# Performance work log

Measured on AMD Instinct MI355X. Metric: run time of the kernel, lower is better.

Reference implementation:

```python
import jax, jax.numpy as jnp
import numpy as np

BN_EPS = 1e-5
KEEP_RATIO = 0.25
MIN_TOPK = 4


def setup_inputs() -> dict:
    key = jax.random.key(0)
    ks = jax.random.split(key, 8)
    B, C, H, W, HID = 32, 768, 32, 32, 96
    x = jax.random.normal(ks[0], (B, C, H, W), dtype=jnp.float32)
    # fan-in scaled weights so score magnitudes stay sane for softmax
    w1 = jax.random.normal(ks[1], (HID, C, 1, 1), dtype=jnp.float32) / np.sqrt(C)
    bn_gamma = jax.random.uniform(ks[2], (HID,), dtype=jnp.float32) + 0.5
    bn_beta = jax.random.normal(ks[3], (HID,), dtype=jnp.float32) * 0.1
    bn_mean = jax.random.normal(ks[4], (HID,), dtype=jnp.float32) * 0.1
    bn_var = jax.random.uniform(ks[5], (HID,), dtype=jnp.float32) + 0.5
    w2 = jax.random.normal(ks[6], (1, HID, 3, 3), dtype=jnp.float32) / np.sqrt(HID * 9)
    b2 = jax.random.normal(ks[7], (1,), dtype=jnp.float32) * 0.1
    return {"x": x, "w1": w1, "bn_gamma": bn_gamma, "bn_beta": bn_beta,
            "bn_mean": bn_mean, "bn_var": bn_var, "w2": w2, "b2": b2}


def reference(x, w1, bn_gamma, bn_beta, bn_mean, bn_var, w2, b2):
    B, C, H, W = x.shape
    N = H * W
    # 1x1 conv (no bias) as channel contraction: [B,C,H,W] x [HID,C] -> [B,HID,H,W]
    h = jnp.einsum('bchw,oc->bohw', x, w1[:, :, 0, 0])
    # BatchNorm in inference mode (running stats)
    scale = (bn_gamma / jnp.sqrt(bn_var + BN_EPS))[None, :, None, None]
    h = h * scale + (bn_beta - bn_mean * bn_gamma / jnp.sqrt(bn_var + BN_EPS))[None, :, None, None]
    h = jax.nn.relu(h)
    # 3x3 conv HID -> 1, padding=1
    score = jax.lax.conv_general_dilated(
        h, w2, window_strides=(1, 1), padding='SAME',
        dimension_numbers=('NCHW', 'OIHW', 'NCHW')) + b2[None, :, None, None]
    s = score.reshape(B, N)
    K = min(max(MIN_TOPK, int(N * KEEP_RATIO)), N)
    top_vals, top_idx = jax.lax.top_k(s, K)  # [B,K] (sorted; weighted sum is order-invariant)
    x_flat = x.reshape(B, C, N)
    sel = jnp.take_along_axis(x_flat, top_idx[:, None, :], axis=2)  # [B,C,K]
    w = jax.nn.softmax(top_vals, axis=1)[:, None, :]               # [B,1,K]
    v = jnp.sum(sel * w, axis=2)                                    # [B,C]
    # dropout p=0.0 -> identity
    return v, score.reshape(B, 1, H, W)
```

## Files before the change

kernel.cpp:

```cpp
#include <hip/hip_runtime.h>
#include <math.h>

#define BB 32
#define CC 768
#define HID 96
#define NPIX 1024
#define KSEL 256
#define BN_EPS_F 1e-5f

typedef __bf16 bf16x8 __attribute__((ext_vector_type(8)));
typedef float f32x4 __attribute__((ext_vector_type(4)));

__device__ __forceinline__ unsigned short f2bf(float f) {
    unsigned u = __float_as_uint(f);
    return (unsigned short)((u + 0x7FFFu + ((u >> 16) & 1u)) >> 16);
}
__device__ __forceinline__ unsigned pack2(float lo, float hi) {
    return (unsigned)f2bf(lo) | ((unsigned)f2bf(hi) << 16);
}

__global__ __launch_bounds__(256) void k0_prep(
    const float* __restrict__ w1, const float* __restrict__ gamma,
    const float* __restrict__ beta, const float* __restrict__ mean,
    const float* __restrict__ var,
    unsigned short* __restrict__ w1b, float* __restrict__ scale,
    float* __restrict__ shift)
{
    int t = threadIdx.x, bk = blockIdx.x;
    if (bk < 72) {
        int idx = (bk * 256 + t) * 4;
        float4 v = *reinterpret_cast<const float4*>(w1 + idx);
        uint2 o;
        o.x = pack2(v.x, v.y);
        o.y = pack2(v.z, v.w);
        *reinterpret_cast<uint2*>(w1b + idx) = o;
    } else if (t < HID) {
        float sc = gamma[t] * rsqrtf(var[t] + BN_EPS_F);
        scale[t] = sc;
        shift[t] = beta[t] - mean[t] * sc;
    }
}

__global__ __launch_bounds__(512, 4) void k1_gemm_mfma(
    const float* __restrict__ x, const unsigned short* __restrict__ w1b,
    const float* __restrict__ scale, const float* __restrict__ shift,
    float* __restrict__ h_out)
{
    __shared__ unsigned Xs[2][32][66];
    __shared__ unsigned short Ws[2][96][68];
    __shared__ float sc_s[HID], sh_s[HID];

    const int t = threadIdx.x;
    const int b = blockIdx.y;
    const int n0 = blockIdx.x * 64;
    const int wave = t >> 6, lane = t & 63;
    const int lm = lane & 15, g = lane >> 4;
    const int wo = wave >> 2, wn = wave & 3;
    const int nB = wn * 16 + lm;
    const int kp = t >> 4, q = t & 15;
    const int nc = q * 4;
    const int wrow = t >> 3, wko = (t & 7) * 8;
    const int wrow2 = (t + 512) >> 3, wko2 = wko;

    if (t < HID) { sc_s[t] = scale[t]; sh_s[t] = shift[t]; }

    f32x4 acc[3];
#pragma unroll
    for (int mt = 0; mt < 3; ++mt) acc[mt] = (f32x4){0.f, 0.f, 0.f, 0.f};

    const float* xbase = x + (size_t)b * CC * NPIX + n0;

    {
        const float* r0 = xbase + (size_t)(2 * kp) * NPIX;
        float4 a4 = *reinterpret_cast<const float4*>(r0 + nc);
        float4 b4 = *reinterpret_cast<const float4*>(r0 + NPIX + nc);
        uint4 pk;
        pk.x = pack2(a4.x, b4.x); pk.y = pack2(a4.y, b4.y);
        pk.z = pack2(a4.z, b4.z); pk.w = pack2(a4.w, b4.w);
        *reinterpret_cast<uint4*>(&Xs[0][kp][nc]) = pk;

        uint4 w0 = *reinterpret_cast<const uint4*>(w1b + (size_t)wrow * CC + wko);
        *reinterpret_cast<uint4*>(&Ws[0][wrow][wko]) = w0;
        if (t < 256) {
            uint4 w1v = *reinterpret_cast<const uint4*>(w1b + (size_t)wrow2 * CC + wko2);
            *reinterpret_cast<uint4*>(&Ws[0][wrow2][wko2]) = w1v;
        }
    }
    __syncthreads();

    int cur = 0;
#pragma unroll 1
    for (int c0 = 0; c0 < CC; c0 += 64) {
        const bool hasNext = (c0 + 64 < CC);
        float4 a4, b4;
        uint4 nw0, nw1;
        if (hasNext) {
            const float* r0 = xbase + (size_t)(c0 + 64 + 2 * kp) * NPIX;
            a4 = *reinterpret_cast<const float4*>(r0 + nc);
            b4 = *reinterpret_cast<const float4*>(r0 + NPIX + nc);
            nw0 = *reinterpret_cast<const uint4*>(
                w1b + (size_t)wrow * CC + c0 + 64 + wko);
            if (t < 256)
                nw1 = *reinterpret_cast<const uint4*>(
                    w1b + (size_t)wrow2 * CC + c0 + 64 + wko2);
        }
#pragma unroll
        for (int h = 0; h < 2; ++h) {
            uint4 bu;
            bu.x = Xs[cur][16 * h + 4 * g + 0][nB];
            bu.y = Xs[cur][16 * h + 4 * g + 1][nB];
            bu.z = Xs[cur][16 * h + 4 * g + 2][nB];
            bu.w = Xs[cur][16 * h + 4 * g + 3][nB];
            bf16x8 bfr = __builtin_bit_cast(bf16x8, bu);
#pragma unroll
            for (int mt = 0; mt < 3; ++mt) {
                uint4 au = *reinterpret_cast<const uint4*>(
                    &Ws[cur][wo * 48 + mt * 16 + lm][h * 32 + g * 8]);
                acc[mt] = __builtin_amdgcn_mfma_f32_16x16x32_bf16(
                    __builtin_bit_cast(bf16x8, au), bfr, acc[mt], 0, 0, 0);
            }
        }
        if (hasNext) {
            uint4 pk;
            pk.x = pack2(a4.x, b4.x); pk.y = pack2(a4.y, b4.y);
            pk.z = pack2(a4.z, b4.z); pk.w = pack2(a4.w, b4.w);
            *reinterpret_cast<uint4*>(&Xs[cur ^ 1][kp][nc]) = pk;
            *reinterpret_cast<uint4*>(&Ws[cur ^ 1][wrow][wko]) = nw0;
            if (t < 256)
                *reinterpret_cast<uint4*>(&Ws[cur ^ 1][wrow2][wko2]) = nw1;
        }
        __syncthreads();
        cur ^= 1;
    }

#pragma unroll
    for (int mt = 0; mt < 3; ++mt) {
#pragma unroll
        for (int r = 0; r < 4; ++r) {
            int o = wo * 48 + mt * 16 + g * 4 + r;
            float v = fmaxf(acc[mt][r] * sc_s[o] + sh_s[o], 0.f);
            h_out[((size_t)b * HID + o) * NPIX + n0 + nB] = v;
        }
    }
}

__global__ __launch_bounds__(128) void k2_conv3x3(
    const float* __restrict__ h_in, const float* __restrict__ w2,
    const float* __restrict__ b2, float* __restrict__ score_out)
{
    __shared__ float hs[16][6][40];
    __shared__ float w2s[HID * 9];

    const int t = threadIdx.x;
    const int ytile = blockIdx.x, b = blockIdx.y;
    const int y = t >> 5, xx = t & 31;
    const int Y = ytile * 4 + y;

    for (int i = t; i < HID * 9; i += 128) w2s[i] = w2[i];

    const float* hb = h_in + (size_t)b * HID * NPIX;
    float acc = 0.f;

    for (int c0 = 0; c0 < HID; c0 += 16) {
        __syncthreads();
        for (int i = t; i < 192; i += 128) {
            int ch = i / 12, rr = (i % 12) >> 1, col = (i & 1) ? 36 : 3;
            hs[ch][rr][col] = 0.f;
        }
#pragma unroll
        for (int i = 0; i < 6; ++i) {
            int idx = t + i * 128;
            int ch = idx / 48, rem = idx % 48;
            int rr = rem >> 3, qq = rem & 7;
            int gy = ytile * 4 - 1 + rr;
            float4 v = (gy >= 0 && gy < 32)
                ? *reinterpret_cast<const float4*>(
                      hb + (size_t)(c0 + ch) * NPIX + gy * 32 + qq * 4)
                : (float4){0.f, 0.f, 0.f, 0.f};
            *reinterpret_cast<float4*>(&hs[ch][rr][4 + qq * 4]) = v;
        }
        __syncthreads();
#pragma unroll
        for (int ch = 0; ch < 16; ++ch) {
            float s = 0.f;
#pragma unroll
            for (int ky = 0; ky < 3; ++ky)
#pragma unroll
                for (int kx = 0; kx < 3; ++kx)
                    s += hs[ch][y + ky][3 + xx + kx] * w2s[(c0 + ch) * 9 + ky * 3 + kx];
            acc += s;
        }
    }
    score_out[b * NPIX + Y * 32 + xx] = acc + b2[0];
}

__global__ __launch_bounds__(256) void k3_topk_softmax(
    const float* __restrict__ score, float* __restrict__ weight)
{
    __shared__ unsigned hist[256];
    __shared__ unsigned wtot[4];
    __shared__ unsigned pcnt16[16];
    __shared__ float redf[4];
    __shared__ unsigned sh_bin, sh_rem;

    const int t = threadIdx.x, b = blockIdx.x;
    const int lane = t & 63, wv = t >> 6;

    float fvals[4];
    unsigned uvals[4];
#pragma unroll
    for (int i = 0; i < 4; ++i) {
        float f = score[b * NPIX + t + 256 * i];
        fvals[i] = f;
        unsigned u = __float_as_uint(f);
        uvals[i] = (u & 0x80000000u) ? ~u : (u | 0x80000000u);
    }

    unsigned prefix = 0, rem = KSEL;
    for (int p = 3; p >= 0; --p) {
        hist[t] = 0;
        __syncthreads();
        const int sh_hi = (p + 1) * 8;
#pragma unroll
        for (int i = 0; i < 4; ++i) {
            unsigned u = uvals[i];
            bool match = (p == 3) || ((u >> sh_hi) == (prefix >> sh_hi));
            if (match) atomicAdd(&hist[(u >> (p * 8)) & 0xffu], 1u);
        }
        __syncthreads();
        unsigned own = hist[t];
        unsigned val = own;
#pragma unroll
        for (int off = 1; off <= 32; off <<= 1) {
            unsigned o2 = __shfl_down(val, off);
            if (lane + off < 64) val += o2;
        }
        if (lane == 0) wtot[wv] = val;
        __syncthreads();
        unsigned suff = val;
        for (int w = wv + 1; w < 4; ++w) suff += wtot[w];
        unsigned nexts = suff - own;
        if (suff >= rem && nexts < rem) { sh_bin = (unsigned)t; sh_rem = rem - nexts; }
        __syncthreads();
        prefix |= (sh_bin << (p * 8));
        rem = sh_rem;
        __syncthreads();
    }
    const unsigned T = prefix, need = rem;

    float m = -INFINITY;
#pragma unroll
    for (int i = 0; i < 4; ++i) m = fmaxf(m, fvals[i]);
#pragma unroll
    for (int off = 32; off >= 1; off >>= 1) m = fmaxf(m, __shfl_xor(m, off));
    if (lane == 0) redf[wv] = m;
    __syncthreads();
    m = fmaxf(fmaxf(redf[0], redf[1]), fmaxf(redf[2], redf[3]));

    unsigned lp[4]; bool eqf[4], gtf[4];
    unsigned long long lmask = (1ULL << lane) - 1ULL;
#pragma unroll
    for (int i = 0; i < 4; ++i) {
        bool eq = (uvals[i] == T);
        eqf[i] = eq; gtf[i] = (uvals[i] > T);
        unsigned long long mk = __ballot(eq);
        lp[i] = (unsigned)__popcll(mk & lmask);
        if (lane == 0) pcnt16[i * 4 + wv] = (unsigned)__popcll(mk);
    }
    __syncthreads();
    unsigned cum = 0, baseArr[4];
#pragma unroll
    for (int ii = 0; ii < 4; ++ii) {
        unsigned b0 = cum;
        for (int w = 0; w < wv; ++w) b0 += pcnt16[ii * 4 + w];
        baseArr[ii] = b0;
        for (int w = 0; w < 4; ++w) cum += pcnt16[ii * 4 + w];
    }
    float evals[4], sumExp = 0.f;
#pragma unroll
    for (int i = 0; i < 4; ++i) {
        bool sel = gtf[i] || (eqf[i] && (baseArr[i] + lp[i]) < need);
        float e = sel ? expf(fvals[i] - m) : 0.f;
        evals[i] = e;
        sumExp += e;
    }
#pragma unroll
    for (int off = 32; off >= 1; off >>= 1) sumExp += __shfl_xor(sumExp, off);
    if (lane == 0) redf[wv] = sumExp;
    __syncthreads();
    float inv = 1.0f / (redf[0] + redf[1] + redf[2] + redf[3]);
#pragma unroll
    for (int i = 0; i < 4; ++i)
        weight[b * NPIX + i * 256 + t] = evals[i] * inv;
}

__global__ __launch_bounds__(256) void k4_weighted_sum(
    const float* __restrict__ x, const float* __restrict__ weight,
    float* __restrict__ v)
{
    __shared__ float wsm[NPIX];
    const int t = threadIdx.x;
    const int b = blockIdx.x / 192, cg = blockIdx.x % 192;

    *reinterpret_cast<float4*>(&wsm[t * 4]) =
        *reinterpret_cast<const float4*>(&weight[b * NPIX + t * 4]);
    __syncthreads();

    const int lane = t & 63, wvv = t >> 6;
    const int c = cg * 4 + wvv;
    const float* xr = x + ((size_t)b * CC + c) * NPIX;

    float acc = 0.f;
#pragma unroll
    for (int j = 0; j < 4; ++j) {
        int off = j * 256 + lane * 4;
        float4 xv = *reinterpret_cast<const float4*>(xr + off);
        float4 wv4 = *reinterpret_cast<const float4*>(&wsm[off]);
        acc += xv.x * wv4.x + xv.y * wv4.y + xv.z * wv4.z + xv.w * wv4.w;
    }
#pragma unroll
    for (int off = 32; off >= 1; off >>= 1) acc += __shfl_xor(acc, off);
    if (lane == 0) v[(size_t)b * CC + c] = acc;
}

extern "C" void kernel_launch(void* const* d_in, const int* in_sizes, int n_in,
                              void* d_out, int out_size, void* d_ws, size_t ws_size,
                              hipStream_t stream)
{
    const float* x     = (const float*)d_in[0];
    const float* w1    = (const float*)d_in[1];
    const float* gamma = (const float*)d_in[2];
    const float* beta  = (const float*)d_in[3];
    const float* mean  = (const float*)d_in[4];
    const float* var   = (const float*)d_in[5];
    const float* w2    = (const float*)d_in[6];
    const float* b2    = (const float*)d_in[7];

    float* out   = (float*)d_out;
    float* vout  = out;
    float* score = out + BB * CC;

    float* h       = (float*)d_ws;
    float* weight  = h + (size_t)BB * HID * NPIX;
    unsigned short* w1b = (unsigned short*)(weight + BB * NPIX);
    float* scale   = (float*)(w1b + HID * CC);
    float* shift   = scale + HID;

    k0_prep<<<73, 256, 0, stream>>>(w1, gamma, beta, mean, var, w1b, scale, shift);
    k1_gemm_mfma<<<dim3(16, BB), 512, 0, stream>>>(x, w1b, scale, shift, h);
    k2_conv3x3<<<dim3(8, BB), 128, 0, stream>>>(h, w2, b2, score);
    k3_topk_softmax<<<BB, 256, 0, stream>>>(score, weight);
    k4_weighted_sum<<<BB * (CC / 4), 256, 0, stream>>>(x, weight, vout);
}
```

Before: 74.09 us.

## Fold weight prep into GEMM and load x directly to registers per lane

After: 74.43 us. Within noise of the previous version (+0.5%).

```diff
diff --git a/kernel.cpp b/kernel.cpp
--- a/kernel.cpp
+++ b/kernel.cpp
@@ -19,35 +19,14 @@
     return (unsigned)f2bf(lo) | ((unsigned)f2bf(hi) << 16);
 }
 
-__global__ __launch_bounds__(256) void k0_prep(
-    const float* __restrict__ w1, const float* __restrict__ gamma,
-    const float* __restrict__ beta, const float* __restrict__ mean,
-    const float* __restrict__ var,
-    unsigned short* __restrict__ w1b, float* __restrict__ scale,
-    float* __restrict__ shift)
-{
-    int t = threadIdx.x, bk = blockIdx.x;
-    if (bk < 72) {
-        int idx = (bk * 256 + t) * 4;
-        float4 v = *reinterpret_cast<const float4*>(w1 + idx);
-        uint2 o;
-        o.x = pack2(v.x, v.y);
-        o.y = pack2(v.z, v.w);
-        *reinterpret_cast<uint2*>(w1b + idx) = o;
-    } else if (t < HID) {
-        float sc = gamma[t] * rsqrtf(var[t] + BN_EPS_F);
-        scale[t] = sc;
-        shift[t] = beta[t] - mean[t] * sc;
-    }
-}
-
 __global__ __launch_bounds__(512, 4) void k1_gemm_mfma(
-    const float* __restrict__ x, const unsigned short* __restrict__ w1b,
-    const float* __restrict__ scale, const float* __restrict__ shift,
+    const float* __restrict__ x, const float* __restrict__ w1,
+    const float* __restrict__ gamma, const float* __restrict__ beta,
+    const float* __restrict__ mean, const float* __restrict__ var,
     float* __restrict__ h_out)
 {
-    __shared__ unsigned Xs[2][32][66];
-    __shared__ unsigned short Ws[2][96][68];
+    constexpr int WSTR = 388;
+    __shared__ unsigned short Ws[96 * WSTR];
     __shared__ float sc_s[HID], sh_s[HID];
 
     const int t = threadIdx.x;
@@ -55,82 +34,83 @@
     const int n0 = blockIdx.x * 64;
     const int wave = t >> 6, lane = t & 63;
     const int lm = lane & 15, g = lane >> 4;
-    const int wo = wave >> 2, wn = wave & 3;
-    const int nB = wn * 16 + lm;
-    const int kp = t >> 4, q = t & 15;
-    const int nc = q * 4;
-    const int wrow = t >> 3, wko = (t & 7) * 8;
-    const int wrow2 = (t + 512) >> 3, wko2 = wko;
-
-    if (t < HID) { sc_s[t] = scale[t]; sh_s[t] = shift[t]; }
+    const int wo = wave & 1, wn = wave >> 1;
+    const int n = n0 + wn * 16 + lm;
+
+    if (t < HID) {
+        float sc = gamma[t] * rsqrtf(var[t] + BN_EPS_F);
+        sc_s[t] = sc;
+        sh_s[t] = beta[t] - mean[t] * sc;
+    }
 
     f32x4 acc[3];
 #pragma unroll
     for (int mt = 0; mt < 3; ++mt) acc[mt] = (f32x4){0.f, 0.f, 0.f, 0.f};
 
-    const float* xbase = x + (size_t)b * CC * NPIX + n0;
-
-    {
-        const float* r0 = xbase + (size_t)(2 * kp) * NPIX;
-        float4 a4 = *reinterpret_cast<const float4*>(r0 + nc);
-        float4 b4 = *reinterpret_cast<const float4*>(r0 + NPIX + nc);
-        uint4 pk;
-        pk.x = pack2(a4.x, b4.x); pk.y = pack2(a4.y, b4.y);
-        pk.z = pack2(a4.z, b4.z); pk.w = pack2(a4.w, b4.w);
-        *reinterpret_cast<uint4*>(&Xs[0][kp][nc]) = pk;
-
-        uint4 w0 = *reinterpret_cast<const uint4*>(w1b + (size_t)wrow * CC + wko);
-        *reinterpret_cast<uint4*>(&Ws[0][wrow][wko]) = w0;
-        if (t < 256) {
-            uint4 w1v = *reinterpret_cast<const uint4*>(w1b + (size_t)wrow2 * CC + wko2);
-            *reinterpret_cast<uint4*>(&Ws[0][wrow2][wko2]) = w1v;
-        }
-    }
-    __syncthreads();
-
-    int cur = 0;
-#pragma unroll 1
-    for (int c0 = 0; c0 < CC; c0 += 64) {
-        const bool hasNext = (c0 + 64 < CC);
-        float4 a4, b4;
-        uint4 nw0, nw1;
-        if (hasNext) {
-            const float* r0 = xbase + (size_t)(c0 + 64 + 2 * kp) * NPIX;
-            a4 = *reinterpret_cast<const float4*>(r0 + nc);
-            b4 = *reinterpret_cast<const float4*>(r0 + NPIX + nc);
-            nw0 = *reinterpret_cast<const uint4*>(
-                w1b + (size_t)wrow * CC + c0 + 64 + wko);
-            if (t < 256)
-                nw1 = *reinterpret_cast<const uint4*>(
-                    w1b + (size_t)wrow2 * CC + c0 + 64 + wko2);
-        }
-#pragma unroll
-        for (int h = 0; h < 2; ++h) {
-            uint4 bu;
-            bu.x = Xs[cur][16 * h + 4 * g + 0][nB];
-            bu.y = Xs[cur][16 * h + 4 * g + 1][nB];
-            bu.z = Xs[cur][16 * h + 4 * g + 2][nB];
-            bu.w = Xs[cur][16 * h + 4 * g + 3][nB];
-            bf16x8 bfr = __builtin_bit_cast(bf16x8, bu);
-#pragma unroll
-            for (int mt = 0; mt < 3; ++mt) {
-                uint4 au = *reinterpret_cast<const uint4*>(
-                    &Ws[cur][wo * 48 + mt * 16 + lm][h * 32 + g * 8]);
-                acc[mt] = __builtin_amdgcn_mfma_f32_16x16x32_bf16(
-                    __builtin_bit_cast(bf16x8, au), bfr, acc[mt], 0, 0, 0);
-            }
-        }
-        if (hasNext) {
-            uint4 pk;
-            pk.x = pack2(a4.x, b4.x); pk.y = pack2(a4.y, b4.y);
-            pk.z = pack2(a4.z, b4.z); pk.w = pack2(a4.w, b4.w);
-            *reinterpret_cast<uint4*>(&Xs[cur ^ 1][kp][nc]) = pk;
-            *reinterpret_cast<uint4*>(&Ws[cur ^ 1][wrow][wko]) = nw0;
-            if (t < 256)
-                *reinterpret_cast<uint4*>(&Ws[cur ^ 1][wrow2][wko2]) = nw1;
-        }
-        __syncthreads();
-        cur ^= 1;
+    const float* xcol = x + (size_t)b * CC * NPIX + (size_t)(g * 8) * NPIX + n;
+
+#define STAGE_W(half) do {                                                    \
+    _Pragma("unroll")                                                         \
+    for (int i = 0; i < 9; ++i) {                                             \
+        int idx = t + i * 512;                                   \
+        int row = idx / 48, k8 = (idx % 48) * 8;                              \
+        const float* src = w1 + (size_t)row * CC + (half) * 384 + k8;         \
+        float4 f0 = *reinterpret_cast<const float4*>(src);                    \
+        float4 f1 = *reinterpret_cast<const float4*>(src + 4);                \
+        uint4 o;                                                              \
+        o.x = pack2(f0.x, f0.y); o.y = pack2(f0.z, f0.w);                     \
+        o.z = pack2(f1.x, f1.y); o.w = pack2(f1.z, f1.w);                     \
+        *reinterpret_cast<uint4*>(&Ws[row * WSTR + k8]) = o;                  \
+    } } while (0)
+
+#define LOADX(dst, ck) do {                                                   \
+    const float* _p = xcol + (size_t)(ck) * 32 * NPIX;                        \
+    _Pragma("unroll")                                                         \
+    for (int j = 0; j < 8; ++j) dst[j] = _p[(size_t)j * NPIX];                \
+    } while (0)
+
+#define PACKX(bu, src) do {                                                   \
+    bu.x = pack2(src[0], src[1]); bu.y = pack2(src[2], src[3]);               \
+    bu.z = pack2(src[4], src[5]); bu.w = pack2(src[6], src[7]); } while (0)
+
+#define CHUNK(ckk, bu) do {                                                   \
+    bf16x8 bfr = __builtin_bit_cast(bf16x8, bu);                              \
+    _Pragma("unroll")                                                         \
+    for (int mt = 0; mt < 3; ++mt) {                                          \
+        uint4 au = *reinterpret_cast<const uint4*>(                           \
+            &Ws[(wo * 48 + mt * 16 + lm) * WSTR + (ckk) * 32 + g * 8]);       \
+        acc[mt] = __builtin_amdgcn_mfma_f32_16x16x32_bf16(                    \
+            __builtin_bit_cast(bf16x8, au), bfr, acc[mt], 0, 0, 0);           \
+    } } while (0)
+
+    float xA[8], xB[8], xC[8], xD[8];
+
+    STAGE_W(0);
+    LOADX(xA, 0); LOADX(xB, 1); LOADX(xC, 2); LOADX(xD, 3);
+    __syncthreads();
+
+#pragma unroll
+    for (int ck = 0; ck < 24; ck += 4) {
+        if (ck == 12) {
+            __syncthreads();
+            STAGE_W(1);
+            __syncthreads();
+        }
+        uint4 bu0; PACKX(bu0, xA);
+        if (ck + 4 < 24) LOADX(xA, ck + 4);
+        CHUNK((ck + 0) % 12, bu0);
+
+        uint4 bu1; PACKX(bu1, xB);
+        if (ck + 5 < 24) LOADX(xB, ck + 5);
+        CHUNK((ck + 1) % 12, bu1);
+
+        uint4 bu2; PACKX(bu2, xC);
+        if (ck + 6 < 24) LOADX(xC, ck + 6);
+        CHUNK((ck + 2) % 12, bu2);
+
+        uint4 bu3; PACKX(bu3, xD);
+        if (ck + 7 < 24) LOADX(xD, ck + 7);
+        CHUNK((ck + 3) % 12, bu3);
     }
 
 #pragma unroll
@@ -139,9 +119,13 @@
         for (int r = 0; r < 4; ++r) {
             int o = wo * 48 + mt * 16 + g * 4 + r;
             float v = fmaxf(acc[mt][r] * sc_s[o] + sh_s[o], 0.f);
-            h_out[((size_t)b * HID + o) * NPIX + n0 + nB] = v;
-        }
-    }
+            h_out[((size_t)b * HID + o) * NPIX + n] = v;
+        }
+    }
+#undef STAGE_W
+#undef LOADX
+#undef PACKX
+#undef CHUNK
 }
 
 __global__ __launch_bounds__(128) void k2_conv3x3(
@@ -340,14 +324,10 @@
     float* vout  = out;
     float* score = out + BB * CC;
 
-    float* h       = (float*)d_ws;
-    float* weight  = h + (size_t)BB * HID * NPIX;
-    unsigned short* w1b = (unsigned short*)(weight + BB * NPIX);
-    float* scale   = (float*)(w1b + HID * CC);
-    float* shift   = scale + HID;
-
-    k0_prep<<<73, 256, 0, stream>>>(w1, gamma, beta, mean, var, w1b, scale, shift);
-    k1_gemm_mfma<<<dim3(16, BB), 512, 0, stream>>>(x, w1b, scale, shift, h);
+    float* h      = (float*)d_ws;
+    float* weight = h + (size_t)BB * HID * NPIX;
+
+    k1_gemm_mfma<<<dim3(16, BB), 512, 0, stream>>>(x, w1, gamma, beta, mean, var, h);
     k2_conv3x3<<<dim3(8, BB), 128, 0, stream>>>(h, w2, b2, score);
     k3_topk_softmax<<<BB, 256, 0, stream>>>(score, weight);
     k4_weighted_sum<<<BB * (CC / 4), 256, 0, stream>>>(x, weight, vout);
```

## Stream x tiles into LDS via global_load_lds with swizzled fp32 layout

Applied to the files above, without the earlier changes.

Result: slower. 77.24 us (+4.3%).

```diff
diff --git a/kernel.cpp b/kernel.cpp
--- a/kernel.cpp
+++ b/kernel.cpp
@@ -10,6 +10,9 @@
 
 typedef __bf16 bf16x8 __attribute__((ext_vector_type(8)));
 typedef float f32x4 __attribute__((ext_vector_type(4)));
+
+typedef const __attribute__((address_space(1))) void* gas_p;
+typedef __attribute__((address_space(3))) void* las_p;
 
 __device__ __forceinline__ unsigned short f2bf(float f) {
     unsigned u = __float_as_uint(f);
@@ -46,7 +49,7 @@
     const float* __restrict__ scale, const float* __restrict__ shift,
     float* __restrict__ h_out)
 {
-    __shared__ unsigned Xs[2][32][66];
+    __shared__ float Xs[2][64 * 64];
     __shared__ unsigned short Ws[2][96][68];
     __shared__ float sc_s[HID], sh_s[HID];
 
@@ -57,10 +60,6 @@
     const int lm = lane & 15, g = lane >> 4;
     const int wo = wave >> 2, wn = wave & 3;
     const int nB = wn * 16 + lm;
-    const int kp = t >> 4, q = t & 15;
-    const int nc = q * 4;
-    const int wrow = t >> 3, wko = (t & 7) * 8;
-    const int wrow2 = (t + 512) >> 3, wko2 = wko;
 
     if (t < HID) { sc_s[t] = scale[t]; sh_s[t] = shift[t]; }
 
@@ -70,65 +69,81 @@
 
     const float* xbase = x + (size_t)b * CC * NPIX + n0;
 
-    {
-        const float* r0 = xbase + (size_t)(2 * kp) * NPIX;
-        float4 a4 = *reinterpret_cast<const float4*>(r0 + nc);
-        float4 b4 = *reinterpret_cast<const float4*>(r0 + NPIX + nc);
-        uint4 pk;
-        pk.x = pack2(a4.x, b4.x); pk.y = pack2(a4.y, b4.y);
-        pk.z = pack2(a4.z, b4.z); pk.w = pack2(a4.w, b4.w);
-        *reinterpret_cast<uint4*>(&Xs[0][kp][nc]) = pk;
-
-        uint4 w0 = *reinterpret_cast<const uint4*>(w1b + (size_t)wrow * CC + wko);
-        *reinterpret_cast<uint4*>(&Ws[0][wrow][wko]) = w0;
-        if (t < 256) {
-            uint4 w1v = *reinterpret_cast<const uint4*>(w1b + (size_t)wrow2 * CC + wko2);
-            *reinterpret_cast<uint4*>(&Ws[0][wrow2][wko2]) = w1v;
-        }
-    }
+    const int cl_0 = wave * 8 + g;
+    const int cl_1 = wave * 8 + 4 + g;
+    const size_t soff0 = (size_t)cl_0 * NPIX + ((lm * 4) ^ (((cl_0 >> 2) & 3) * 8));
+    const size_t soff1 = (size_t)cl_1 * NPIX + ((lm * 4) ^ (((cl_1 >> 2) & 3) * 8));
+    const int ldst0 = (wave * 8) * 64;
+    const int ldst1 = (wave * 8 + 4) * 64;
+
+    const int sA = nB ^ (((2 * g) & 3) * 8);
+    const int sB = nB ^ (((2 * g + 1) & 3) * 8);
+
+#define ISSUE_X(buf, c0next) do {                                             \
+    __builtin_amdgcn_global_load_lds(                                         \
+        (gas_p)(xbase + (size_t)(c0next) * NPIX + soff0),                     \
+        (las_p)(&Xs[buf][ldst0]), 16, 0, 0);                                  \
+    __builtin_amdgcn_global_load_lds(                                         \
+        (gas_p)(xbase + (size_t)(c0next) * NPIX + soff1),                     \
+        (las_p)(&Xs[buf][ldst1]), 16, 0, 0);                                  \
+    } while (0)
+
+#define LOADW(c0n) do {                                                       \
+    wr0 = *reinterpret_cast<const uint4*>(                                    \
+        w1b + (size_t)(t >> 3) * CC + (c0n) + (t & 7) * 8);                   \
+    if (t < 256)                                                              \
+        wr1 = *reinterpret_cast<const uint4*>(                                \
+            w1b + (size_t)((512 + t) >> 3) * CC + (c0n) + (t & 7) * 8);       \
+    } while (0)
+
+#define WRITEW(buf) do {                                                      \
+    *reinterpret_cast<uint4*>(&Ws[buf][t >> 3][(t & 7) * 8]) = wr0;           \
+    if (t < 256)                                                              \
+        *reinterpret_cast<uint4*>(&Ws[buf][(512 + t) >> 3][(t & 7) * 8]) = wr1;\
+    } while (0)
+
+#define COMPUTE(buf) do {                                                     \
+    const float* Xc = Xs[buf];                                                \
+    _Pragma("unroll")                                                         \
+    for (int h = 0; h < 2; ++h) {                                             \
+        float f0 = Xc[(h * 32 + g * 8 + 0) * 64 + sA];                        \
+        float f1 = Xc[(h * 32 + g * 8 + 1) * 64 + sA];                        \
+        float f2 = Xc[(h * 32 + g * 8 + 2) * 64 + sA];                        \
+        float f3 = Xc[(h * 32 + g * 8 + 3) * 64 + sA];                        \
+        float f4 = Xc[(h * 32 + g * 8 + 4) * 64 + sB];                        \
+        float f5 = Xc[(h * 32 + g * 8 + 5) * 64 + sB];                        \
+        float f6 = Xc[(h * 32 + g * 8 + 6) * 64 + sB];                        \
+        float f7 = Xc[(h * 32 + g * 8 + 7) * 64 + sB];                        \
+        uint4 bu;                                                             \
+        bu.x = pack2(f0, f1); bu.y = pack2(f2, f3);                           \
+        bu.z = pack2(f4, f5); bu.w = pack2(f6, f7);                           \
+        bf16x8 bfr = __builtin_bit_cast(bf16x8, bu);                          \
+        _Pragma("unroll")                                                     \
+        for (int mt = 0; mt < 3; ++mt) {                                      \
+            uint4 au = *reinterpret_cast<const uint4*>(                       \
+                &Ws[buf][wo * 48 + mt * 16 + lm][h * 32 + g * 8]);            \
+            acc[mt] = __builtin_amdgcn_mfma_f32_16x16x32_bf16(                \
+                __builtin_bit_cast(bf16x8, au), bfr, acc[mt], 0, 0, 0);       \
+        }                                                                     \
+    } } while (0)
+
+    uint4 wr0, wr1;
+
+    ISSUE_X(0, 0);
+    LOADW(0);
+    WRITEW(0);
     __syncthreads();
 
     int cur = 0;
 #pragma unroll 1
     for (int c0 = 0; c0 < CC; c0 += 64) {
         const bool hasNext = (c0 + 64 < CC);
-        float4 a4, b4;
-        uint4 nw0, nw1;
         if (hasNext) {
-            const float* r0 = xbase + (size_t)(c0 + 64 + 2 * kp) * NPIX;
-            a4 = *reinterpret_cast<const float4*>(r0 + nc);
-            b4 = *reinterpret_cast<const float4*>(r0 + NPIX + nc);
-            nw0 = *reinterpret_cast<const uint4*>(
-                w1b + (size_t)wrow * CC + c0 + 64 + wko);
-            if (t < 256)
-                nw1 = *reinterpret_cast<const uint4*>(
-                    w1b + (size_t)wrow2 * CC + c0 + 64 + wko2);
-        }
-#pragma unroll
-        for (int h = 0; h < 2; ++h) {
-            uint4 bu;
-            bu.x = Xs[cur][16 * h + 4 * g + 0][nB];
-            bu.y = Xs[cur][16 * h + 4 * g + 1][nB];
-            bu.z = Xs[cur][16 * h + 4 * g + 2][nB];
-            bu.w = Xs[cur][16 * h + 4 * g + 3][nB];
-            bf16x8 bfr = __builtin_bit_cast(bf16x8, bu);
-#pragma unroll
-            for (int mt = 0; mt < 3; ++mt) {
-                uint4 au = *reinterpret_cast<const uint4*>(
-                    &Ws[cur][wo * 48 + mt * 16 + lm][h * 32 + g * 8]);
-                acc[mt] = __builtin_amdgcn_mfma_f32_16x16x32_bf16(
-                    __builtin_bit_cast(bf16x8, au), bfr, acc[mt], 0, 0, 0);
-            }
-        }
-        if (hasNext) {
-            uint4 pk;
-            pk.x = pack2(a4.x, b4.x); pk.y = pack2(a4.y, b4.y);
-            pk.z = pack2(a4.z, b4.z); pk.w = pack2(a4.w, b4.w);
-            *reinterpret_cast<uint4*>(&Xs[cur ^ 1][kp][nc]) = pk;
-            *reinterpret_cast<uint4*>(&Ws[cur ^ 1][wrow][wko]) = nw0;
-            if (t < 256)
-                *reinterpret_cast<uint4*>(&Ws[cur ^ 1][wrow2][wko2]) = nw1;
-        }
+            ISSUE_X(cur ^ 1, c0 + 64);
+            LOADW(c0 + 64);
+        }
+        COMPUTE(cur);
+        if (hasNext) WRITEW(cur ^ 1);
         __syncthreads();
         cur ^= 1;
     }
@@ -142,6 +157,10 @@
             h_out[((size_t)b * HID + o) * NPIX + n0 + nB] = v;
         }
     }
+#undef ISSUE_X
+#undef LOADW
+#undef WRITEW
+#undef COMPUTE
 }
 
 __global__ __launch_bounds__(128) void k2_conv3x3(
```
